# Kernel tuning notes

Measured on AMD Instinct MI355X. Metric: run time of the kernel, lower is better.

The kernel has to match this reference:

```python
import jax, jax.numpy as jnp
import numpy as np

H = 8  # nhead
EPS = 1e-5


def _ln(x, g, b):
    mu = x.mean(-1, keepdims=True)
    var = ((x - mu) ** 2).mean(-1, keepdims=True)
    return (x - mu) / jnp.sqrt(var + EPS) * g + b


def _mha(q_in, kv_in, w_qkv, b_qkv, w_o, b_o, mask):
    # PyTorch nn.MultiheadAttention with packed in_proj: rows [Wq; Wk; Wv], y = x @ W.T + b
    d = q_in.shape[-1]
    hd = d // H
    wq, wk, wv = jnp.split(w_qkv, 3, axis=0)
    bq, bk, bv = jnp.split(b_qkv, 3)
    B, Lq = q_in.shape[0], q_in.shape[1]
    Lk = kv_in.shape[1]
    q = (q_in @ wq.T + bq).reshape(B, Lq, H, hd).transpose(0, 2, 1, 3)
    k = (kv_in @ wk.T + bk).reshape(B, Lk, H, hd).transpose(0, 2, 1, 3)
    v = (kv_in @ wv.T + bv).reshape(B, Lk, H, hd).transpose(0, 2, 1, 3)
    s = jnp.einsum('bhqd,bhkd->bhqk', q, k) * np.float32(1.0 / np.sqrt(hd))
    if mask is not None:
        s = s + mask  # additive causal mask, (Lq, Lk) broadcast
    a = jax.nn.softmax(s, axis=-1)
    o = jnp.einsum('bhqk,bhkd->bhqd', a, v).transpose(0, 2, 1, 3).reshape(B, Lq, d)
    return o @ w_o.T + b_o


def _forward(z, target_ids, tok_emb, pos_emb, lp_w, lp_b, lp_ln_g, lp_ln_b,
             sa_qkv_w, sa_qkv_b, sa_out_w, sa_out_b,
             ca_qkv_w, ca_qkv_b, ca_out_w, ca_out_b,
             ln1_g, ln1_b, ln2_g, ln2_b, ln3_g, ln3_b,
             ff1_w, ff1_b, ff2_w, ff2_b, op_w, op_b):
    B, L = target_ids.shape
    # latent_proj: Linear -> GELU (exact) -> LayerNorm; (B, 1, d) memory
    mem = jax.nn.gelu(z @ lp_w.T + lp_b, approximate=False)
    mem = _ln(mem, lp_ln_g, lp_ln_b)[:, None, :]
    # token + positional embedding
    x = tok_emb[target_ids] + pos_emb[jnp.arange(L)][None, :, :]
    # causal additive mask (upper triangle = -inf)
    causal = jnp.where(jnp.tril(jnp.ones((L, L), dtype=bool)), 0.0, -1e9).astype(x.dtype)
    n_layers = sa_qkv_w.shape[0]
    for i in range(n_layers):  # post-norm TransformerDecoderLayer (norm_first=False)
        x = _ln(x + _mha(x, x, sa_qkv_w[i], sa_qkv_b[i], sa_out_w[i], sa_out_b[i], causal), ln1_g[i], ln1_b[i])
        x = _ln(x + _mha(x, mem, ca_qkv_w[i], ca_qkv_b[i], ca_out_w[i], ca_out_b[i], None), ln2_g[i], ln2_b[i])
        ff = jax.nn.relu(x @ ff1_w[i].T + ff1_b[i]) @ ff2_w[i].T + ff2_b[i]
        x = _ln(x + ff, ln3_g[i], ln3_b[i])
    return x @ op_w.T + op_b  # (B, L, vocab)


def setup_inputs() -> dict:
    B, L, D, LAT, V, NL = 32, 128, 512, 256, 50257, 4
    DF = 4 * D
    key = jax.random.key(0)
    ks = jax.random.split(key, 20)
    s = 0.02
    n = lambda k, shp: jax.random.normal(k, shp, dtype=jnp.float32) * s
    return {
        'z': jax.random.normal(ks[0], (B, LAT), dtype=jnp.float32),
        'target_ids': jax.random.randint(ks[1], (B, L), 0, V),
        'tok_emb': n(ks[2], (V, D)),
        'pos_emb': n(ks[3], (L, D)),
        'lp_w': n(ks[4], (D, LAT)), 'lp_b': jnp.zeros((D,)),
        'lp_ln_g': jnp.ones((D,)), 'lp_ln_b': jnp.zeros((D,)),
        'sa_qkv_w': n(ks[5], (NL, 3 * D, D)), 'sa_qkv_b': jnp.zeros((NL, 3 * D)),
        'sa_out_w': n(ks[6], (NL, D, D)), 'sa_out_b': jnp.zeros((NL, D)),
        'ca_qkv_w': n(ks[7], (NL, 3 * D, D)), 'ca_qkv_b': jnp.zeros((NL, 3 * D)),
        'ca_out_w': n(ks[8], (NL, D, D)), 'ca_out_b': jnp.zeros((NL, D)),
        'ln1_g': jnp.ones((NL, D)), 'ln1_b': jnp.zeros((NL, D)),
        'ln2_g': jnp.ones((NL, D)), 'ln2_b': jnp.zeros((NL, D)),
        'ln3_g': jnp.ones((NL, D)), 'ln3_b': jnp.zeros((NL, D)),
        'ff1_w': n(ks[9], (NL, DF, D)), 'ff1_b': jnp.zeros((NL, DF)),
        'ff2_w': n(ks[10], (NL, D, DF)), 'ff2_b': jnp.zeros((NL, D)),
        'op_w': n(ks[11], (V, D)), 'op_b': jnp.zeros((V,)),
    }


def reference(z, target_ids, tok_emb, pos_emb, lp_w, lp_b, lp_ln_g, lp_ln_b,
              sa_qkv_w, sa_qkv_b, sa_out_w, sa_out_b,
              ca_qkv_w, ca_qkv_b, ca_out_w, ca_out_b,
              ln1_g, ln1_b, ln2_g, ln2_b, ln3_g, ln3_b,
              ff1_w, ff1_b, ff2_w, ff2_b, op_w, op_b):
    return _forward(z, target_ids, tok_emb, pos_emb, lp_w, lp_b, lp_ln_g, lp_ln_b,
                    sa_qkv_w, sa_qkv_b, sa_out_w, sa_out_b,
                    ca_qkv_w, ca_qkv_b, ca_out_w, ca_out_b,
                    ln1_g, ln1_b, ln2_g, ln2_b, ln3_g, ln3_b,
                    ff1_w, ff1_b, ff2_w, ff2_b, op_w, op_b)
```

## Files before the change

kernel.cpp:

```cpp
#include <hip/hip_runtime.h>
#include <math.h>

typedef __attribute__((ext_vector_type(8))) short short8;
typedef __attribute__((ext_vector_type(4))) float f32x4;
typedef __attribute__((ext_vector_type(4))) float f4;
typedef __attribute__((ext_vector_type(4))) unsigned short us4;
typedef unsigned short u16;

#define Bn 32
#define Ln 128
#define Dn 512
#define LATn 256
#define Vn 50257
#define VPAD 50304
#define DFn 2048
#define Hn 8
#define HDn 64

#define GLD(src, dst) __builtin_amdgcn_global_load_lds( \
    (const __attribute__((address_space(1))) unsigned int*)(src), \
    (__attribute__((address_space(3))) unsigned int*)(dst), 16, 0, 0)

__device__ __forceinline__ u16 f2bf(float f) {
  union { float f; unsigned u; } v; v.f = f;
  unsigned r = 0x7FFFu + ((v.u >> 16) & 1u);
  return (u16)((v.u + r) >> 16);
}
__device__ __forceinline__ float bf2f(u16 u) {
  union { unsigned u; float f; } v; v.u = ((unsigned)u) << 16;
  return v.f;
}

__global__ __launch_bounds__(256)
void k_cvt_all(const float* __restrict__ s0, const float* __restrict__ s1,
               const float* __restrict__ s2, const float* __restrict__ s3,
               const float* __restrict__ s4, us4* __restrict__ dst) {
  const int C0 = 786432;
  const int C1 = 1048576;
  const int C2 = 2097152;
  const int C3 = 3145728;
  const int C4 = 9584640;
  const int OPN4 = 6432896;
  int i = blockIdx.x * blockDim.x + threadIdx.x;
  int stride = gridDim.x * blockDim.x;
  for (; i < C4; i += stride) {
    const f4* src; int off; bool valid = true;
    if (i < C0)      { src = (const f4*)s0; off = i; }
    else if (i < C1) { src = (const f4*)s1; off = i - C0; }
    else if (i < C2) { src = (const f4*)s2; off = i - C1; }
    else if (i < C3) { src = (const f4*)s3; off = i - C2; }
    else             { src = (const f4*)s4; off = i - C3; valid = off < OPN4; }
    us4 o;
    if (valid) {
      f4 v = src[off];
      o[0] = f2bf(v[0]); o[1] = f2bf(v[1]); o[2] = f2bf(v[2]); o[3] = f2bf(v[3]);
    } else { o[0] = 0; o[1] = 0; o[2] = 0; o[3] = 0; }
    dst[i] = o;
  }
}

__global__ __launch_bounds__(256)
void k_latent_mem(const float* __restrict__ z, const float* __restrict__ lp_w,
                  const float* __restrict__ lp_b, const float* __restrict__ g,
                  const float* __restrict__ be, float* __restrict__ mem) {
  __shared__ float zs[LATn];
  __shared__ float red[16];
  int b = blockIdx.x, t = threadIdx.x;
  zs[t] = z[b * LATn + t];
  __syncthreads();
  float h[2];
  #pragma unroll
  for (int j = 0; j < 2; j++) {
    int oj = t + j * 256;
    const float* w = lp_w + (size_t)oj * LATn;
    float s0 = 0, s1 = 0, s2 = 0, s3 = 0;
    for (int k = 0; k < LATn; k += 4) {
      s0 += zs[k] * w[k]; s1 += zs[k+1] * w[k+1];
      s2 += zs[k+2] * w[k+2]; s3 += zs[k+3] * w[k+3];
    }
    float x = s0 + s1 + s2 + s3 + lp_b[oj];
    h[j] = 0.5f * x * (1.0f + erff(x * 0.70710678118654752f));
  }
  float sum = h[0] + h[1], sq = h[0]*h[0] + h[1]*h[1];
  for (int off = 32; off; off >>= 1) {
    sum += __shfl_down(sum, off, 64);
    sq  += __shfl_down(sq,  off, 64);
  }
  int lane = t & 63, wid = t >> 6;
  if (!lane) { red[wid] = sum; red[8 + wid] = sq; }
  __syncthreads();
  float ts = red[0] + red[1] + red[2] + red[3];
  float tq = red[8] + red[9] + red[10] + red[11];
  float mu = ts * (1.0f / Dn);
  float var = tq * (1.0f / Dn) - mu * mu;
  float rstd = rsqrtf(fmaxf(var, 0.0f) + 1e-5f);
  #pragma unroll
  for (int j = 0; j < 2; j++) {
    int oj = t + j * 256;
    mem[b * Dn + oj] = (h[j] - mu) * rstd * g[oj] + be[oj];
  }
}

__global__ __launch_bounds__(256)
void k_ca(const float* __restrict__ mem, const float* __restrict__ ca_qkv_w,
          const float* __restrict__ ca_qkv_b, const float* __restrict__ ca_out_w,
          const float* __restrict__ ca_out_b, float* __restrict__ ca_add) {
  int blk = blockIdx.x;
  int i = blk >> 5, b = blk & 31, t = threadIdx.x;
  __shared__ float ms[Dn];
  __shared__ float vs[Dn];
  ms[t] = mem[b * Dn + t];
  ms[t + 256] = mem[b * Dn + t + 256];
  __syncthreads();
  const float* wv = ca_qkv_w + ((size_t)i * 1536 + 1024) * Dn;
  const float* bv = ca_qkv_b + i * 1536 + 1024;
  for (int j = t; j < Dn; j += 256) {
    const float* w = wv + (size_t)j * Dn;
    float s0 = 0, s1 = 0, s2 = 0, s3 = 0;
    for (int k = 0; k < Dn; k += 4) {
      s0 += ms[k]*w[k]; s1 += ms[k+1]*w[k+1]; s2 += ms[k+2]*w[k+2]; s3 += ms[k+3]*w[k+3];
    }
    vs[j] = s0 + s1 + s2 + s3 + bv[j];
  }
  __syncthreads();
  const float* wo = ca_out_w + (size_t)i * Dn * Dn;
  const float* bo = ca_out_b + i * Dn;
  for (int j = t; j < Dn; j += 256) {
    const float* w = wo + (size_t)j * Dn;
    float s0 = 0, s1 = 0, s2 = 0, s3 = 0;
    for (int k = 0; k < Dn; k += 4) {
      s0 += vs[k]*w[k]; s1 += vs[k+1]*w[k+1]; s2 += vs[k+2]*w[k+2]; s3 += vs[k+3]*w[k+3];
    }
    ca_add[((size_t)i * Bn + b) * Dn + j] = s0 + s1 + s2 + s3 + bo[j];
  }
}

__global__ __launch_bounds__(128)
void k_embed(const int* __restrict__ ids, const float* __restrict__ tok,
             const float* __restrict__ pos, float* __restrict__ X,
             u16* __restrict__ Xb) {
  int r = blockIdx.x;
  int l = r & (Ln - 1);
  int id = ids[r];
  int c = threadIdx.x * 4;
  f4 te = *(const f4*)&tok[(size_t)id * Dn + c];
  f4 pe = *(const f4*)&pos[(size_t)l * Dn + c];
  f4 v = te + pe;
  *(f4*)&X[(size_t)r * Dn + c] = v;
  us4 o = { f2bf(v[0]), f2bf(v[1]), f2bf(v[2]), f2bf(v[3]) };
  *(us4*)&Xb[(size_t)r * Dn + c] = o;
}

__global__ __launch_bounds__(128)
void k_add_ln(float* __restrict__ X, u16* __restrict__ Xb,
              const u16* __restrict__ Y, const float* __restrict__ g,
              const float* __restrict__ be) {
  int r = blockIdx.x, t = threadIdx.x;
  int c = t * 4;
  f4 x = *(const f4*)&X[(size_t)r * Dn + c];
  us4 yb = *(const us4*)&Y[(size_t)r * Dn + c];
  f4 v;
  v[0] = x[0] + bf2f(yb[0]); v[1] = x[1] + bf2f(yb[1]);
  v[2] = x[2] + bf2f(yb[2]); v[3] = x[3] + bf2f(yb[3]);
  float sum = v[0] + v[1] + v[2] + v[3];
  float sq = v[0]*v[0] + v[1]*v[1] + v[2]*v[2] + v[3]*v[3];
  for (int off = 32; off; off >>= 1) {
    sum += __shfl_down(sum, off, 64);
    sq  += __shfl_down(sq,  off, 64);
  }
  __shared__ float red[4];
  int lane = t & 63, w = t >> 6;
  if (!lane) { red[w] = sum; red[2 + w] = sq; }
  __syncthreads();
  sum = red[0] + red[1]; sq = red[2] + red[3];
  float mu = sum * (1.0f / Dn);
  float var = sq * (1.0f / Dn) - mu * mu;
  float rstd = rsqrtf(fmaxf(var, 0.0f) + 1e-5f);
  f4 gg = *(const f4*)&g[c];
  f4 bb = *(const f4*)&be[c];
  f4 o = (v - mu) * rstd * gg + bb;
  *(f4*)&X[(size_t)r * Dn + c] = o;
  us4 ob = { f2bf(o[0]), f2bf(o[1]), f2bf(o[2]), f2bf(o[3]) };
  *(us4*)&Xb[(size_t)r * Dn + c] = ob;
}

__global__ __launch_bounds__(128)
void k_add_ln12(float* __restrict__ X, u16* __restrict__ Xb,
                const u16* __restrict__ Y, const float* __restrict__ CA,
                const float* __restrict__ g1, const float* __restrict__ b1,
                const float* __restrict__ g2, const float* __restrict__ b2) {
  int r = blockIdx.x, t = threadIdx.x;
  int c = t * 4;
  __shared__ float red[8];
  int lane = t & 63, w = t >> 6;
  f4 x = *(const f4*)&X[(size_t)r * Dn + c];
  us4 yb = *(const us4*)&Y[(size_t)r * Dn + c];
  f4 v;
  v[0] = x[0] + bf2f(yb[0]); v[1] = x[1] + bf2f(yb[1]);
  v[2] = x[2] + bf2f(yb[2]); v[3] = x[3] + bf2f(yb[3]);
  float sum = v[0] + v[1] + v[2] + v[3];
  float sq = v[0]*v[0] + v[1]*v[1] + v[2]*v[2] + v[3]*v[3];
  for (int off = 32; off; off >>= 1) {
    sum += __shfl_down(sum, off, 64);
    sq  += __shfl_down(sq,  off, 64);
  }
  if (!lane) { red[w] = sum; red[2 + w] = sq; }
  __syncthreads();
  sum = red[0] + red[1]; sq = red[2] + red[3];
  float mu = sum * (1.0f / Dn);
  float var = sq * (1.0f / Dn) - mu * mu;
  float rstd = rsqrtf(fmaxf(var, 0.0f) + 1e-5f);
  f4 g1v = *(const f4*)&g1[c];
  f4 b1v = *(const f4*)&b1[c];
  f4 o1 = (v - mu) * rstd * g1v + b1v;
  f4 ca = *(const f4*)&CA[(size_t)(r >> 7) * Dn + c];
  f4 v2 = o1 + ca;
  float sum2 = v2[0] + v2[1] + v2[2] + v2[3];
  float sq2 = v2[0]*v2[0] + v2[1]*v2[1] + v2[2]*v2[2] + v2[3]*v2[3];
  for (int off = 32; off; off >>= 1) {
    sum2 += __shfl_down(sum2, off, 64);
    sq2  += __shfl_down(sq2,  off, 64);
  }
  if (!lane) { red[4 + w] = sum2; red[6 + w] = sq2; }
  __syncthreads();
  sum2 = red[4] + red[5]; sq2 = red[6] + red[7];
  float mu2 = sum2 * (1.0f / Dn);
  float var2 = sq2 * (1.0f / Dn) - mu2 * mu2;
  float rstd2 = rsqrtf(fmaxf(var2, 0.0f) + 1e-5f);
  f4 g2v = *(const f4*)&g2[c];
  f4 b2v = *(const f4*)&b2[c];
  f4 o2 = (v2 - mu2) * rstd2 * g2v + b2v;
  *(f4*)&X[(size_t)r * Dn + c] = o2;
  us4 ob = { f2bf(o2[0]), f2bf(o2[1]), f2bf(o2[2]), f2bf(o2[3]) };
  *(us4*)&Xb[(size_t)r * Dn + c] = ob;
}

__global__ __launch_bounds__(256, 1)
void k_attn_m(const u16* __restrict__ QKV, u16* __restrict__ Ob) {
  constexpr int QS = 0;
  constexpr int KS = 9216;
  constexpr int SFB = 36864;
  constexpr int VTB = 36864 + 66048;
  constexpr int MXB = VTB + 17408;
  constexpr int LXB = MXB + 1024;
  __shared__ __align__(16) char smem[LXB + 1024];
  u16* U = (u16*)smem;
  float* Sf = (float*)(smem + SFB);
  u16* Vt = (u16*)(smem + VTB);
  float* Mx = (float*)(smem + MXB);
  float* Lx = (float*)(smem + LXB);

  int bh = blockIdx.x, b = bh >> 3, h = bh & 7;
  int tid = threadIdx.x, lane = tid & 63, wid = tid >> 6;
  int r = tid & 127, half = tid >> 7;

  {
    const u16* qk = QKV + (size_t)(b * 128 + r) * 1536 + (half ? 512 : 0) + h * 64;
    u16* dst = U + (half ? KS : QS) + r * 72;
    #pragma unroll
    for (int i = 0; i < 64; i += 8)
      *(short8*)(dst + i) = *(const short8*)(qk + i);
    const u16* vsrc = QKV + (size_t)(b * 128 + r) * 1536 + 1024 + h * 64 + half * 32;
    #pragma unroll
    for (int i = 0; i < 32; i += 8) {
      short8 v = *(const short8*)(vsrc + i);
      #pragma unroll
      for (int j = 0; j < 8; j++)
        Vt[(half * 32 + i + j) * 136 + r] = (u16)v[j];
    }
  }
  __syncthreads();

  int qb = wid * 32;
  int fr = lane & 15, qk8 = (lane >> 4) * 8, qrl = (lane >> 4) * 4;
  f32x4 sacc[2][8] = {};
  #pragma unroll
  for (int s = 0; s < 2; s++) {
    short8 av[2], bv[8];
    #pragma unroll
    for (int mi = 0; mi < 2; mi++)
      av[mi] = *(const short8*)(U + QS + (qb + mi * 16 + fr) * 72 + s * 32 + qk8);
    #pragma unroll
    for (int nj = 0; nj < 8; nj++)
      bv[nj] = *(const short8*)(U + KS + (nj * 16 + fr) * 72 + s * 32 + qk8);
    #pragma unroll
    for (int mi = 0; mi < 2; mi++)
      #pragma unroll
      for (int nj = 0; nj < 8; nj++)
        sacc[mi][nj] = __builtin_amdgcn_mfma_f32_16x16x32_bf16(
            av[mi], bv[nj], sacc[mi][nj], 0, 0, 0);
  }
  #pragma unroll
  for (int mi = 0; mi < 2; mi++)
    #pragma unroll
    for (int nj = 0; nj < 8; nj++)
      #pragma unroll
      for (int g = 0; g < 4; g++) {
        int q = qb + mi * 16 + qrl + g;
        int k = nj * 16 + fr;
        Sf[q * 129 + k] = (k <= q) ? sacc[mi][nj][g] * 0.125f : -1e30f;
      }
  __syncthreads();

  int kr = half * 64;
  float m = -1e30f;
  for (int k = 0; k < 64; k++) m = fmaxf(m, Sf[r * 129 + kr + k]);
  Mx[half * 128 + r] = m;
  __syncthreads();
  float mm = fmaxf(Mx[r], Mx[128 + r]);
  float l = 0.0f;
  for (int k = 0; k < 64; k++) {
    float p = __expf(Sf[r * 129 + kr + k] - mm);
    Sf[r * 129 + kr + k] = p;
    l += p;
  }
  Lx[half * 128 + r] = l;
  __syncthreads();
  float linv = 1.0f / (Lx[r] + Lx[128 + r]);
  #pragma unroll
  for (int kc = 0; kc < 8; kc++) {
    short8 pv;
    #pragma unroll
    for (int j = 0; j < 8; j++)
      pv[j] = (short)f2bf(Sf[r * 129 + kr + kc * 8 + j] * linv);
    *(short8*)(U + r * 136 + kr + kc * 8) = pv;
  }
  __syncthreads();

  f32x4 oacc[2][4] = {};
  #pragma unroll
  for (int ks = 0; ks < 4; ks++) {
    short8 av[2], bv[4];
    #pragma unroll
    for (int mi = 0; mi < 2; mi++)
      av[mi] = *(const short8*)(U + (qb + mi * 16 + fr) * 136 + ks * 32 + qk8);
    #pragma unroll
    for (int nj = 0; nj < 4; nj++)
      bv[nj] = *(const short8*)(Vt + (nj * 16 + fr) * 136 + ks * 32 + qk8);
    #pragma unroll
    for (int mi = 0; mi < 2; mi++)
      #pragma unroll
      for (int nj = 0; nj < 4; nj++)
        oacc[mi][nj] = __builtin_amdgcn_mfma_f32_16x16x32_bf16(
            av[mi], bv[nj], oacc[mi][nj], 0, 0, 0);
  }
  #pragma unroll
  for (int mi = 0; mi < 2; mi++)
    #pragma unroll
    for (int nj = 0; nj < 4; nj++)
      #pragma unroll
      for (int g = 0; g < 4; g++) {
        int q = qb + mi * 16 + qrl + g;
        int d = nj * 16 + fr;
        Ob[(size_t)(b * 128 + q) * 512 + h * 64 + d] = f2bf(oacc[mi][nj][g]);
      }
}

template <int EPI, int BNT>
__global__ __launch_bounds__(256, (BNT == 128 ? 2 : 3))
void k_gemm_bt(const u16* __restrict__ A, const u16* __restrict__ Bw,
               const float* __restrict__ bias, void* __restrict__ Cout,
               int gm, int N, int K, int ldc) {
  constexpr int NREP = BNT / 32;
  constexpr int ASTRIDE = 128 * 64;
  constexpr int BSTRIDE = BNT * 64;
  constexpr int TSTRIDE = BNT + 4;
  constexpr int NLA = 4;
  constexpr int NLB = BNT / 32;
  __shared__ __align__(16) char smem[(ASTRIDE + BSTRIDE) * 4];
  u16* As = (u16*)smem;
  u16* Bs = (u16*)(smem + ASTRIDE * 4);
  float* Ts = (float*)smem;

  int lin = blockIdx.x;
  int bm = lin % gm, bn = lin / gm;
  int tid = threadIdx.x, lane = tid & 63, wid = tid >> 6;
  int wr = wid >> 1, wc = wid & 1;
  int fr = lane & 15, q = lane >> 4;
  f32x4 acc[4][NREP] = {};

  auto stage = [&](int it) {
    int buf = it & 1;
    #pragma unroll
    for (int l = 0; l < NLA; l++) {
      int c = tid + l * 256;
      int row = c >> 3;
      int kcg = (c & 7) ^ (row & 7);
      GLD(A + (size_t)(bm * 128 + row) * K + it * 64 + kcg * 8,
          (char*)(As + buf * ASTRIDE) + c * 16);
    }
    #pragma unroll
    for (int l = 0; l < NLB; l++) {
      int c = tid + l * 256;
      int row = c >> 3;
      int kcg = (c & 7) ^ (row & 7);
      GLD(Bw + (size_t)(bn * BNT + row) * K + it * 64 + kcg * 8,
          (char*)(Bs + buf * BSTRIDE) + c * 16);
    }
  };

  int nt = K >> 6;
  stage(0);
  for (int it = 0; it < nt; ++it) {
    int cur = it & 1;
    if (it + 1 < nt) {
      stage(it + 1);
      if constexpr (BNT == 128) asm volatile("s_waitcnt vmcnt(8)" ::: "memory");
      else                      asm volatile("s_waitcnt vmcnt(6)" ::: "memory");
    } else {
      asm volatile("s_waitcnt vmcnt(0)" ::: "memory");
    }
    __builtin_amdgcn_sched_barrier(0);
    __builtin_amdgcn_s_barrier();
    __builtin_amdgcn_sched_barrier(0);
    short8 av[2][4], bv[2][NREP];
    #pragma unroll
    for (int s = 0; s < 2; s++) {
      #pragma unroll
      for (int mi = 0; mi < 4; mi++) {
        int row = wr * 64 + mi * 16 + fr;
        int phys = (s * 4 + q) ^ (row & 7);
        av[s][mi] = *(const short8*)&As[cur * ASTRIDE + row * 64 + phys * 8];
      }
      #pragma unroll
      for (int nj = 0; nj < NREP; nj++) {
        int row = wc * (BNT / 2) + nj * 16 + fr;
        int phys = (s * 4 + q) ^ (row & 7);
        bv[s][nj] = *(const short8*)&Bs[cur * BSTRIDE + row * 64 + phys * 8];
      }
    }
    #pragma unroll
    for (int s = 0; s < 2; s++)
      #pragma unroll
      for (int mi = 0; mi < 4; mi++)
        #pragma unroll
        for (int nj = 0; nj < NREP; nj++)
          acc[mi][nj] = __builtin_amdgcn_mfma_f32_16x16x32_bf16(
              av[s][mi], bv[s][nj], acc[mi][nj], 0, 0, 0);
    asm volatile("s_waitcnt lgkmcnt(0)" ::: "memory");
    __builtin_amdgcn_sched_barrier(0);
    __builtin_amdgcn_s_barrier();
    __builtin_amdgcn_sched_barrier(0);
  }

  float bb[NREP];
  #pragma unroll
  for (int nj = 0; nj < NREP; nj++) {
    int cg = bn * BNT + wc * (BNT / 2) + nj * 16 + fr;
    bb[nj] = (cg < N) ? bias[cg] : 0.0f;
  }
  int rl0 = (lane >> 4) * 4;
  #pragma unroll
  for (int mi = 0; mi < 4; mi++) {
    #pragma unroll
    for (int nj = 0; nj < NREP; nj++) {
      int colL = wc * (BNT / 2) + nj * 16 + fr;
      #pragma unroll
      for (int r = 0; r < 4; r++)
        Ts[(wr * 16 + rl0 + r) * TSTRIDE + colL] = acc[mi][nj][r] + bb[nj];
    }
    __syncthreads();
    constexpr int ITERS = (32 * BNT) / 256;
    #pragma unroll
    for (int i = 0; i < ITERS; i++) {
      int flat = i * 256 + tid;
      int rowf = flat / BNT, col = flat % BNT;
      float v = Ts[rowf * TSTRIDE + col];
      int row_g = bm * 128 + (rowf >> 4) * 64 + mi * 16 + (rowf & 15);
      int col_g = bn * BNT + col;
      size_t off = (size_t)row_g * ldc + col_g;
      if (EPI == 0) {
        if (col_g < N) ((float*)Cout)[off] = v;
      } else if (EPI == 1) {
        ((u16*)Cout)[off] = f2bf(fmaxf(v, 0.0f));
      } else {
        ((u16*)Cout)[off] = f2bf(v);
      }
    }
    if (mi < 3) __syncthreads();
  }
}

__global__ __launch_bounds__(512, 2)
void k_gemm_v256(const u16* __restrict__ A, const u16* __restrict__ Bw,
                 const float* __restrict__ bias, float* __restrict__ Cout,
                 int gm, int N, int K, int ldc) {
  constexpr int ASTRIDE = 256 * 64;
  constexpr int BSTRIDE = 256 * 64;
  constexpr int TSTRIDE = 256 + 4;
  __shared__ __align__(16) char smem[(ASTRIDE + BSTRIDE) * 4];
  u16* As = (u16*)smem;
  u16* Bs = (u16*)(smem + ASTRIDE * 4);
  float* Ts = (float*)smem;

  int lin = blockIdx.x;
  int bm = lin % gm, bn = lin / gm;
  int tid = threadIdx.x, lane = tid & 63, wid = tid >> 6;
  int wr = wid >> 2, wc = wid & 3;
  int fr = lane & 15, q = lane >> 4;
  f32x4 acc[8][4] = {};

  auto stage = [&](int it) {
    int buf = it & 1;
    #pragma unroll
    for (int l = 0; l < 4; l++) {
      int c = tid + l * 512;
      int row = c >> 3;
      int kcg = (c & 7) ^ (row & 7);
      GLD(A + (size_t)(bm * 256 + row) * K + it * 64 + kcg * 8,
          (char*)(As + buf * ASTRIDE) + c * 16);
    }
    #pragma unroll
    for (int l = 0; l < 4; l++) {
      int c = tid + l * 512;
      int row = c >> 3;
      int rowg = bn * 256 + row;
      if (rowg > VPAD - 1) rowg = VPAD - 1;
      int kcg = (c & 7) ^ (row & 7);
      GLD(Bw + (size_t)rowg * K + it * 64 + kcg * 8,
          (char*)(Bs + buf * BSTRIDE) + c * 16);
    }
  };

  int nt = K >> 6;
  stage(0);
  for (int it = 0; it < nt; ++it) {
    int cur = it & 1;
    if (it + 1 < nt) {
      stage(it + 1);
      asm volatile("s_waitcnt vmcnt(8)" ::: "memory");
    } else {
      asm volatile("s_waitcnt vmcnt(0)" ::: "memory");
    }
    __builtin_amdgcn_sched_barrier(0);
    __builtin_amdgcn_s_barrier();
    __builtin_amdgcn_sched_barrier(0);
    #pragma unroll
    for (int s = 0; s < 2; s++) {
      short8 av[8], bv[4];
      #pragma unroll
      for (int mi = 0; mi < 8; mi++) {
        int row = wr * 128 + mi * 16 + fr;
        int phys = (s * 4 + q) ^ (row & 7);
        av[mi] = *(const short8*)&As[cur * ASTRIDE + row * 64 + phys * 8];
      }
      #pragma unroll
      for (int nj = 0; nj < 4; nj++) {
        int row = wc * 64 + nj * 16 + fr;
        int phys = (s * 4 + q) ^ (row & 7);
        bv[nj] = *(const short8*)&Bs[cur * BSTRIDE + row * 64 + phys * 8];
      }
      #pragma unroll
      for (int mi = 0; mi < 8; mi++)
        #pragma unroll
        for (int nj = 0; nj < 4; nj++)
          acc[mi][nj] = __builtin_amdgcn_mfma_f32_16x16x32_bf16(
              av[mi], bv[nj], acc[mi][nj], 0, 0, 0);
    }
    asm volatile("s_waitcnt lgkmcnt(0)" ::: "memory");
    __builtin_amdgcn_sched_barrier(0);
    __builtin_amdgcn_s_barrier();
    __builtin_amdgcn_sched_barrier(0);
  }

  float bb[4];
  #pragma unroll
  for (int nj = 0; nj < 4; nj++) {
    int cg = bn * 256 + wc * 64 + nj * 16 + fr;
    bb[nj] = (cg < N) ? bias[cg] : 0.0f;
  }
  int rl0 = (lane >> 4) * 4;
  #pragma unroll
  for (int mi = 0; mi < 8; mi++) {
    #pragma unroll
    for (int nj = 0; nj < 4; nj++) {
      int colL = wc * 64 + nj * 16 + fr;
      #pragma unroll
      for (int r = 0; r < 4; r++)
        Ts[(wr * 16 + rl0 + r) * TSTRIDE + colL] = acc[mi][nj][r] + bb[nj];
    }
    __syncthreads();
    #pragma unroll
    for (int i = 0; i < 16; i++) {
      int flat = i * 512 + tid;
      int rowf = flat >> 8, col = flat & 255;
      float v = Ts[rowf * TSTRIDE + col];
      int row_g = bm * 256 + (rowf >> 4) * 128 + mi * 16 + (rowf & 15);
      int col_g = bn * 256 + col;
      if (col_g < N)
        Cout[(size_t)row_g * ldc + col_g] = v;
    }
    if (mi < 7) __syncthreads();
  }
}

extern "C" void kernel_launch(void* const* d_in, const int* in_sizes, int n_in,
                              void* d_out, int out_size, void* d_ws, size_t ws_size,
                              hipStream_t stream) {
  const float* z        = (const float*)d_in[0];
  const int*   ids      = (const int*)d_in[1];
  const float* tok      = (const float*)d_in[2];
  const float* pos      = (const float*)d_in[3];
  const float* lp_w     = (const float*)d_in[4];
  const float* lp_b     = (const float*)d_in[5];
  const float* lp_g     = (const float*)d_in[6];
  const float* lp_be    = (const float*)d_in[7];
  const float* sa_qkv_w = (const float*)d_in[8];
  const float* sa_qkv_b = (const float*)d_in[9];
  const float* sa_out_w = (const float*)d_in[10];
  const float* sa_out_b = (const float*)d_in[11];
  const float* ca_qkv_w = (const float*)d_in[12];
  const float* ca_qkv_b = (const float*)d_in[13];
  const float* ca_out_w = (const float*)d_in[14];
  const float* ca_out_b = (const float*)d_in[15];
  const float* ln1_g    = (const float*)d_in[16];
  const float* ln1_b    = (const float*)d_in[17];
  const float* ln2_g    = (const float*)d_in[18];
  const float* ln2_b    = (const float*)d_in[19];
  const float* ln3_g    = (const float*)d_in[20];
  const float* ln3_b    = (const float*)d_in[21];
  const float* ff1_w    = (const float*)d_in[22];
  const float* ff1_b    = (const float*)d_in[23];
  const float* ff2_w    = (const float*)d_in[24];
  const float* ff2_b    = (const float*)d_in[25];
  const float* op_w     = (const float*)d_in[26];
  const float* op_b     = (const float*)d_in[27];

  char* ws = (char*)d_ws;
  float* X      = (float*)(ws + 0);
  u16*   Yb     = (u16*)(ws + 8388608);
  u16*   QKVb   = (u16*)(ws + 16777216);
  u16*   Xb     = (u16*)(ws + 29360128);
  u16*   Ob     = (u16*)(ws + 33554432);
  u16*   H1b    = (u16*)(ws + 37748736);
  float* mem    = (float*)(ws + 54525952);
  float* ca_add = (float*)(ws + 54657024);
  u16*   Wa     = (u16*)(ws + 55050240);

  u16* Wqkv = Wa;
  u16* Wout = Wa + 3145728;
  u16* Wff1 = Wa + 4194304;
  u16* Wff2 = Wa + 8388608;
  u16* Wop  = Wa + 12582912;

  k_latent_mem<<<Bn, 256, 0, stream>>>(z, lp_w, lp_b, lp_g, lp_be, mem);
  k_ca<<<4 * Bn, 256, 0, stream>>>(mem, ca_qkv_w, ca_qkv_b, ca_out_w, ca_out_b, ca_add);
  k_embed<<<Bn * Ln, 128, 0, stream>>>(ids, tok, pos, X, Xb);
  k_cvt_all<<<2048, 256, 0, stream>>>(sa_qkv_w, sa_out_w, ff1_w, ff2_w, op_w,
                                      (us4*)Wa);

  const int M = Bn * Ln;
  for (int i = 0; i < 4; i++) {
    k_gemm_bt<2, 128><<<32 * 12, 256, 0, stream>>>(
        Xb, Wqkv + (size_t)i * 1536 * Dn, sa_qkv_b + i * 1536, QKVb, 32, 1536, Dn, 1536);
    k_attn_m<<<Bn * Hn, 256, 0, stream>>>(QKVb, Ob);
    k_gemm_bt<2, 64><<<32 * 8, 256, 0, stream>>>(
        Ob, Wout + (size_t)i * Dn * Dn, sa_out_b + i * Dn, Yb, 32, Dn, Dn, Dn);
    k_add_ln12<<<M, 128, 0, stream>>>(X, Xb, Yb, ca_add + (size_t)i * Bn * Dn,
                                      ln1_g + i * Dn, ln1_b + i * Dn,
                                      ln2_g + i * Dn, ln2_b + i * Dn);
    k_gemm_bt<1, 128><<<32 * 16, 256, 0, stream>>>(
        Xb, Wff1 + (size_t)i * DFn * Dn, ff1_b + i * DFn, H1b, 32, DFn, Dn, DFn);
    k_gemm_bt<2, 64><<<32 * 8, 256, 0, stream>>>(
        H1b, Wff2 + (size_t)i * Dn * DFn, ff2_b + i * Dn, Yb, 32, Dn, DFn, Dn);
    k_add_ln<<<M, 128, 0, stream>>>(X, Xb, Yb, ln3_g + i * Dn, ln3_b + i * Dn);
  }

  k_gemm_v256<<<16 * 197, 512, 0, stream>>>(
      Xb, Wop, op_b, (float*)d_out, 16, Vn, Dn, Vn);
}
```

Before: 819.2 us.

## Retile vocab GEMM to 256x192 with triple-buffered B and interleaved loads

The output-projection GEMM tile changes from 256x256 to 256x192 columns. The B tile is now triple-buffered and staged two k-steps ahead, and the A loads are split into halves issued in the middle of the MFMA phases. Per-subtile waits, s_setprio around the MFMA bursts and extra barriers try to overlap global loads with compute and cut the wait at the top of each loop. The 192-column tile gives 262 column blocks, which also changes tile-count granularity against N, at the cost of more barriers and lower arithmetic intensity per B byte.

```diff
diff --git a/kernel.cpp b/kernel.cpp
--- a/kernel.cpp
+++ b/kernel.cpp
@@ -482,15 +482,15 @@
 }
 
 __global__ __launch_bounds__(512, 2)
-void k_gemm_v256(const u16* __restrict__ A, const u16* __restrict__ Bw,
-                 const float* __restrict__ bias, float* __restrict__ Cout,
-                 int gm, int N, int K, int ldc) {
-  constexpr int ASTRIDE = 256 * 64;
-  constexpr int BSTRIDE = 256 * 64;
-  constexpr int TSTRIDE = 256 + 4;
-  __shared__ __align__(16) char smem[(ASTRIDE + BSTRIDE) * 4];
+void k_gemm_v8(const u16* __restrict__ A, const u16* __restrict__ Bw,
+               const float* __restrict__ bias, float* __restrict__ Cout,
+               int gm, int N, int K, int ldc) {
+  constexpr int AST = 256 * 64;
+  constexpr int BST = 192 * 64;
+  constexpr int TSTRIDE = 192 + 4;
+  __shared__ __align__(16) char smem[AST * 2 * 2 + BST * 3 * 2];
   u16* As = (u16*)smem;
-  u16* Bs = (u16*)(smem + ASTRIDE * 4);
+  u16* Bs = (u16*)(smem + AST * 4);
   float* Ts = (float*)smem;
 
   int lin = blockIdx.x;
@@ -498,95 +498,101 @@
   int tid = threadIdx.x, lane = tid & 63, wid = tid >> 6;
   int wr = wid >> 2, wc = wid & 3;
   int fr = lane & 15, q = lane >> 4;
-  f32x4 acc[8][4] = {};
-
-  auto stage = [&](int it) {
-    int buf = it & 1;
-    #pragma unroll
-    for (int l = 0; l < 4; l++) {
+  f32x4 acc[8][3] = {};
+  int nt = K >> 6;
+
+  auto stageAh = [&](int j, int half) {
+    int sl = j & 1;
+    #pragma unroll
+    for (int l = 0; l < 2; l++) {
+      int c = tid + l * 512;
+      int row = half * 128 + (c >> 3);
+      int kcg = (c & 7) ^ (row & 7);
+      GLD(A + (size_t)(bm * 256 + row) * K + j * 64 + kcg * 8,
+          (char*)(As + sl * AST) + (half * 1024 + c) * 16);
+    }
+  };
+  auto stageB = [&](int j) {
+    int sl = j % 3;
+    #pragma unroll
+    for (int l = 0; l < 3; l++) {
       int c = tid + l * 512;
       int row = c >> 3;
       int kcg = (c & 7) ^ (row & 7);
-      GLD(A + (size_t)(bm * 256 + row) * K + it * 64 + kcg * 8,
-          (char*)(As + buf * ASTRIDE) + c * 16);
-    }
-    #pragma unroll
-    for (int l = 0; l < 4; l++) {
-      int c = tid + l * 512;
-      int row = c >> 3;
-      int rowg = bn * 256 + row;
-      if (rowg > VPAD - 1) rowg = VPAD - 1;
-      int kcg = (c & 7) ^ (row & 7);
-      GLD(Bw + (size_t)rowg * K + it * 64 + kcg * 8,
-          (char*)(Bs + buf * BSTRIDE) + c * 16);
+      GLD(Bw + (size_t)(bn * 192 + row) * K + j * 64 + kcg * 8,
+          (char*)(Bs + sl * BST) + c * 16);
     }
   };
 
-  int nt = K >> 6;
-  stage(0);
-  for (int it = 0; it < nt; ++it) {
-    int cur = it & 1;
-    if (it + 1 < nt) {
-      stage(it + 1);
-      asm volatile("s_waitcnt vmcnt(8)" ::: "memory");
-    } else {
-      asm volatile("s_waitcnt vmcnt(0)" ::: "memory");
-    }
+  stageB(0);
+  if (nt > 1) stageB(1);
+  stageAh(0, 0); stageAh(0, 1);
+
+  for (int kt = 0; kt < nt; ++kt) {
+    int adb = kt & 1, bsl = kt % 3;
+    if (kt + 1 < nt) stageAh(kt + 1, 0);
+    if (kt == 0 && nt > 1)      asm volatile("s_waitcnt vmcnt(2)" ::: "memory");
+    else if (kt + 1 < nt)       asm volatile("s_waitcnt vmcnt(5)" ::: "memory");
+    else                        asm volatile("s_waitcnt vmcnt(0)" ::: "memory");
     __builtin_amdgcn_sched_barrier(0);
     __builtin_amdgcn_s_barrier();
     __builtin_amdgcn_sched_barrier(0);
-    #pragma unroll
-    for (int s = 0; s < 2; s++) {
-      short8 av[8], bv[4];
+    short8 av[2][8];
+    #pragma unroll
+    for (int s = 0; s < 2; s++)
       #pragma unroll
       for (int mi = 0; mi < 8; mi++) {
         int row = wr * 128 + mi * 16 + fr;
-        int phys = (s * 4 + q) ^ (row & 7);
-        av[mi] = *(const short8*)&As[cur * ASTRIDE + row * 64 + phys * 8];
+        av[s][mi] = *(const short8*)
+            &As[adb * AST + row * 64 + ((s * 4 + q) ^ (row & 7)) * 8];
       }
-      #pragma unroll
-      for (int nj = 0; nj < 4; nj++) {
-        int row = wc * 64 + nj * 16 + fr;
-        int phys = (s * 4 + q) ^ (row & 7);
-        bv[nj] = *(const short8*)&Bs[cur * BSTRIDE + row * 64 + phys * 8];
+    #pragma unroll
+    for (int p = 0; p < 3; p++) {
+      if (p == 1) { if (kt + 1 < nt) stageAh(kt + 1, 1); }
+      if (p == 2) { if (kt + 2 < nt) stageB(kt + 2); }
+      #pragma unroll
+      for (int s = 0; s < 2; s++) {
+        int row = wc * 48 + p * 16 + fr;
+        short8 bv = *(const short8*)
+            &Bs[bsl * BST + row * 64 + ((s * 4 + q) ^ (row & 7)) * 8];
+        asm volatile("s_waitcnt lgkmcnt(0)" ::: "memory");
+        __builtin_amdgcn_sched_barrier(0);
+        __builtin_amdgcn_s_setprio(1);
+        #pragma unroll
+        for (int mi = 0; mi < 8; mi++)
+          acc[mi][p] = __builtin_amdgcn_mfma_f32_16x16x32_bf16(
+              av[s][mi], bv, acc[mi][p], 0, 0, 0);
+        __builtin_amdgcn_s_setprio(0);
       }
-      #pragma unroll
-      for (int mi = 0; mi < 8; mi++)
-        #pragma unroll
-        for (int nj = 0; nj < 4; nj++)
-          acc[mi][nj] = __builtin_amdgcn_mfma_f32_16x16x32_bf16(
-              av[mi], bv[nj], acc[mi][nj], 0, 0, 0);
-    }
-    asm volatile("s_waitcnt lgkmcnt(0)" ::: "memory");
-    __builtin_amdgcn_sched_barrier(0);
-    __builtin_amdgcn_s_barrier();
-    __builtin_amdgcn_sched_barrier(0);
-  }
-
-  float bb[4];
-  #pragma unroll
-  for (int nj = 0; nj < 4; nj++) {
-    int cg = bn * 256 + wc * 64 + nj * 16 + fr;
+      __builtin_amdgcn_s_barrier();
+      __builtin_amdgcn_sched_barrier(0);
+    }
+  }
+
+  float bb[3];
+  #pragma unroll
+  for (int nj = 0; nj < 3; nj++) {
+    int cg = bn * 192 + wc * 48 + nj * 16 + fr;
     bb[nj] = (cg < N) ? bias[cg] : 0.0f;
   }
   int rl0 = (lane >> 4) * 4;
   #pragma unroll
   for (int mi = 0; mi < 8; mi++) {
     #pragma unroll
-    for (int nj = 0; nj < 4; nj++) {
-      int colL = wc * 64 + nj * 16 + fr;
+    for (int nj = 0; nj < 3; nj++) {
+      int colL = wc * 48 + nj * 16 + fr;
       #pragma unroll
       for (int r = 0; r < 4; r++)
         Ts[(wr * 16 + rl0 + r) * TSTRIDE + colL] = acc[mi][nj][r] + bb[nj];
     }
     __syncthreads();
     #pragma unroll
-    for (int i = 0; i < 16; i++) {
+    for (int i = 0; i < 12; i++) {
       int flat = i * 512 + tid;
-      int rowf = flat >> 8, col = flat & 255;
+      int rowf = flat / 192, col = flat % 192;
       float v = Ts[rowf * TSTRIDE + col];
       int row_g = bm * 256 + (rowf >> 4) * 128 + mi * 16 + (rowf & 15);
-      int col_g = bn * 256 + col;
+      int col_g = bn * 192 + col;
       if (col_g < N)
         Cout[(size_t)row_g * ldc + col_g] = v;
     }
@@ -666,6 +672,6 @@
     k_add_ln<<<M, 128, 0, stream>>>(X, Xb, Yb, ln3_g + i * Dn, ln3_b + i * Dn);
   }
 
-  k_gemm_v256<<<16 * 197, 512, 0, stream>>>(
+  k_gemm_v8<<<16 * 262, 512, 0, stream>>>(
       Xb, Wop, op_b, (float*)d_out, 16, Vn, Dn, Vn);
 }
```

Result: slower. 862.8 us (+5.3%).
